# Performance work log

Measured on AMD Instinct MI355X. Metric: run time of the kernel, lower is better.

The kernel has to match this reference:

```python
import jax, jax.numpy as jnp
import numpy as np


def setup_inputs() -> dict:
    key = jax.random.key(0)
    k1, k2 = jax.random.split(key)
    B, IN, OUT = 8192, 4096, 2048
    x = jax.random.normal(k1, (B, IN), dtype=jnp.float32)
    # kaiming_normal_ on a (1, IN, OUT) tensor: fan_in = IN*OUT (torch treats dim0 as out-ch),
    # but the exact init scale is irrelevant for a correctness baseline; use std ~ sqrt(2/fan_in).
    std = np.sqrt(2.0 / (IN * OUT)).astype(np.float32)
    weight = jax.random.normal(k2, (1, IN, OUT), dtype=jnp.float32) * std
    return {"x": x, "weight": weight}


def reference(x, weight):
    # Faithful math: out[b, o] = sqrt(sum_i (x[b, i] - w[i, o])^2)
    # avoids the [B, IN, OUT] broadcast intermediate the torch code materializes).
    w = weight[0]                                   # [IN, OUT]
    x2 = jnp.sum(x * x, axis=1, keepdims=True)      # [B, 1]
    w2 = jnp.sum(w * w, axis=0, keepdims=True)      # [1, OUT]
    xw = jnp.matmul(x, w)                           # [B, OUT]
    d2 = x2 - 2.0 * xw + w2
    return jnp.sqrt(jnp.maximum(d2, 0.0))           # clamp tiny negative roundoff
```

## Files before the change

### kernel.cpp

```cpp
#include <hip/hip_runtime.h>


static constexpr int Mdim = 8192;
static constexpr int Ndim = 2048;
static constexpr int Kdim = 4096;

#define TILE_M 128
#define TILE_N 128
#define TILE_K 32

typedef float f32x4 __attribute__((ext_vector_type(4)));
typedef short s16x8 __attribute__((ext_vector_type(8)));
typedef __attribute__((address_space(3))) unsigned int lds_u32;
typedef const __attribute__((address_space(1))) unsigned int glb_u32;

__device__ __forceinline__ unsigned short f2bf(float f) {
    unsigned int u = __float_as_uint(f);
    return (unsigned short)((u + 0x7fffu + ((u >> 16) & 1u)) >> 16);
}

__global__ void prep_x_kernel(const float* __restrict__ x,
                              unsigned short* __restrict__ xb,
                              float* __restrict__ x2) {
    const int row = blockIdx.x;
    const int tid = threadIdx.x;
    const float4* xr = (const float4*)(x + (size_t)row * Kdim);
    ushort4* xo = (ushort4*)(xb + (size_t)row * Kdim);
    float ss = 0.f;
#pragma unroll
    for (int j = 0; j < 4; ++j) {
        float4 v = xr[j * 256 + tid];
        ss += v.x * v.x + v.y * v.y + v.z * v.z + v.w * v.w;
        ushort4 o;
        o.x = f2bf(v.x); o.y = f2bf(v.y); o.z = f2bf(v.z); o.w = f2bf(v.w);
        xo[j * 256 + tid] = o;
    }
#pragma unroll
    for (int d = 32; d >= 1; d >>= 1) ss += __shfl_down(ss, d, 64);
    __shared__ float ps[4];
    if ((tid & 63) == 0) ps[tid >> 6] = ss;
    __syncthreads();
    if (tid == 0) x2[row] = ps[0] + ps[1] + ps[2] + ps[3];
}

__global__ void prep_wt_kernel(const float* __restrict__ w,
                               unsigned short* __restrict__ wb,
                               float* __restrict__ w2) {
    __shared__ float t[64][65];
    const int tid = threadIdx.x;
    const int c0 = blockIdx.x * 64;
    const int r0 = blockIdx.y * 64;
#pragma unroll
    for (int p = 0; p < 4; ++p) {
        const int r = p * 16 + (tid >> 4);
        const int c = (tid & 15) * 4;
        float4 v = *(const float4*)(w + (size_t)(r0 + r) * Ndim + c0 + c);
        t[r][c] = v.x; t[r][c + 1] = v.y; t[r][c + 2] = v.z; t[r][c + 3] = v.w;
    }
    __syncthreads();
#pragma unroll
    for (int p = 0; p < 2; ++p) {
        const int o  = p * 32 + (tid >> 3);
        const int kc = (tid & 7) * 8;
        float ss = 0.f;
        ushort4 a, b;
        float v;
        v = t[kc + 0][o]; ss += v * v; a.x = f2bf(v);
        v = t[kc + 1][o]; ss += v * v; a.y = f2bf(v);
        v = t[kc + 2][o]; ss += v * v; a.z = f2bf(v);
        v = t[kc + 3][o]; ss += v * v; a.w = f2bf(v);
        v = t[kc + 4][o]; ss += v * v; b.x = f2bf(v);
        v = t[kc + 5][o]; ss += v * v; b.y = f2bf(v);
        v = t[kc + 6][o]; ss += v * v; b.z = f2bf(v);
        v = t[kc + 7][o]; ss += v * v; b.w = f2bf(v);
        ushort4* dst = (ushort4*)(wb + (size_t)(c0 + o) * Kdim + r0 + kc);
        dst[0] = a; dst[1] = b;
        ss += __shfl_xor(ss, 1, 64);
        ss += __shfl_xor(ss, 2, 64);
        ss += __shfl_xor(ss, 4, 64);
        if ((tid & 7) == 0) atomicAdd(&w2[c0 + o], ss);
    }
}

__global__ __launch_bounds__(256, 2) void gemm_dist_kernel(
    const unsigned short* __restrict__ Xb,
    const unsigned short* __restrict__ Wb,
    const float* __restrict__ x2,
    const float* __restrict__ w2,
    float* __restrict__ out)
{
    __shared__ __align__(16) unsigned char lds[2][16384];
    const int tid = threadIdx.x;
    const int lane = tid & 63;
    const int wid = tid >> 6;
    const int wr = wid >> 1, wc = wid & 1;

    const int nt_n = Ndim / TILE_N;
    const int nwg = (Mdim / TILE_M) * nt_n;
    const int q = nwg >> 3;
    const int swz = (blockIdx.x & 7) * q + (blockIdx.x >> 3);
    const int bm0 = (swz / nt_n) * TILE_M;
    const int bn0 = (swz % nt_n) * TILE_N;

    int srcA[2], srcB[2];
#pragma unroll
    for (int j = 0; j < 2; ++j) {
        int chunk = j * 256 + tid;
        int row = chunk >> 2;
        int scir = (chunk ^ row) & 3;
        srcA[j] = (bm0 + row) * Kdim + scir * 8;
        srcB[j] = (bn0 + row) * Kdim + scir * 8;
    }

    int aoff[4], boff[4];
#pragma unroll
    for (int m = 0; m < 4; ++m) {
        int ra = wr * 64 + m * 16 + (lane & 15);
        aoff[m] = ra * 64 + ((((lane >> 4) ^ ra) & 3) << 4);
        int rb = wc * 64 + m * 16 + (lane & 15);
        boff[m] = 8192 + rb * 64 + ((((lane >> 4) ^ rb) & 3) << 4);
    }

    f32x4 acc[4][4];
#pragma unroll
    for (int m = 0; m < 4; ++m)
#pragma unroll
        for (int n = 0; n < 4; ++n) acc[m][n] = (f32x4){0.f, 0.f, 0.f, 0.f};

    auto stage = [&](int bufi, int kt) {
        const unsigned short* ga0 = Xb + srcA[0] + kt * TILE_K;
        const unsigned short* ga1 = Xb + srcA[1] + kt * TILE_K;
        const unsigned short* gb0 = Wb + srcB[0] + kt * TILE_K;
        const unsigned short* gb1 = Wb + srcB[1] + kt * TILE_K;
        unsigned char* base = &lds[bufi][0];
        __builtin_amdgcn_global_load_lds((glb_u32*)ga0, (lds_u32*)(base + wid * 1024), 16, 0, 0);
        __builtin_amdgcn_global_load_lds((glb_u32*)ga1, (lds_u32*)(base + 4096 + wid * 1024), 16, 0, 0);
        __builtin_amdgcn_global_load_lds((glb_u32*)gb0, (lds_u32*)(base + 8192 + wid * 1024), 16, 0, 0);
        __builtin_amdgcn_global_load_lds((glb_u32*)gb1, (lds_u32*)(base + 8192 + 4096 + wid * 1024), 16, 0, 0);
    };

    stage(0, 0);
    __syncthreads();

    const int NT = Kdim / TILE_K;
    for (int kt = 0; kt < NT; ++kt) {
        const int cur = kt & 1;
        if (kt + 1 < NT) stage(cur ^ 1, kt + 1);
        const unsigned char* buf = &lds[cur][0];
        s16x8 af[4], bf[4];
#pragma unroll
        for (int m = 0; m < 4; ++m) af[m] = *(const s16x8*)(buf + aoff[m]);
#pragma unroll
        for (int n = 0; n < 4; ++n) bf[n] = *(const s16x8*)(buf + boff[n]);
#pragma unroll
        for (int m = 0; m < 4; ++m)
#pragma unroll
            for (int n = 0; n < 4; ++n)
                acc[m][n] = __builtin_amdgcn_mfma_f32_16x16x32_bf16(af[m], bf[n], acc[m][n], 0, 0, 0);
        __syncthreads();
    }

    const int col0 = bn0 + wc * 64 + (lane & 15);
    const int rb0 = bm0 + wr * 64 + ((lane >> 4) << 2);
    float w2v[4];
#pragma unroll
    for (int n = 0; n < 4; ++n) w2v[n] = w2[col0 + n * 16];
#pragma unroll
    for (int m = 0; m < 4; ++m) {
#pragma unroll
        for (int i = 0; i < 4; ++i) {
            const int row = rb0 + m * 16 + i;
            const float xv = x2[row];
#pragma unroll
            for (int n = 0; n < 4; ++n) {
                float d2 = xv - 2.f * acc[m][n][i] + w2v[n];
                out[(size_t)row * Ndim + col0 + n * 16] = sqrtf(fmaxf(d2, 0.f));
            }
        }
    }
}

__global__ __launch_bounds__(256) void fallback_dist_kernel(
    const float* __restrict__ x, const float* __restrict__ w, float* __restrict__ out)
{
    __shared__ float xs[16][65];
    __shared__ float wsd[16][65];
    const int tid = threadIdx.x;
    const int m0 = blockIdx.y * 64;
    const int n0 = blockIdx.x * 64;
    const int tx = tid & 15, ty = tid >> 4;
    float acc[4][4] = {};
    for (int k0 = 0; k0 < Kdim; k0 += 16) {
        __syncthreads();
#pragma unroll
        for (int p = 0; p < 4; ++p) {
            int idx = p * 256 + tid;
            int kk = idx >> 6, c = idx & 63;
            xs[kk][c] = x[(size_t)(m0 + c) * Kdim + k0 + kk];
            wsd[kk][c] = w[(size_t)(k0 + kk) * Ndim + n0 + c];
        }
        __syncthreads();
#pragma unroll
        for (int kk = 0; kk < 16; ++kk) {
            float a[4], b[4];
#pragma unroll
            for (int i = 0; i < 4; ++i) a[i] = xs[kk][ty * 4 + i];
#pragma unroll
            for (int j = 0; j < 4; ++j) b[j] = wsd[kk][tx * 4 + j];
#pragma unroll
            for (int i = 0; i < 4; ++i)
#pragma unroll
                for (int j = 0; j < 4; ++j) {
                    float d = a[i] - b[j];
                    acc[i][j] += d * d;
                }
        }
    }
#pragma unroll
    for (int i = 0; i < 4; ++i)
#pragma unroll
        for (int j = 0; j < 4; ++j)
            out[(size_t)(m0 + ty * 4 + i) * Ndim + n0 + tx * 4 + j] = sqrtf(acc[i][j]);
}

extern "C" void kernel_launch(void* const* d_in, const int* in_sizes, int n_in,
                              void* d_out, int out_size, void* d_ws, size_t ws_size,
                              hipStream_t stream) {
    const float* x = (const float*)d_in[0];
    const float* w = (const float*)d_in[1];
    float* out = (float*)d_out;
    char* ws = (char*)d_ws;

    const size_t xb_bytes = (size_t)Mdim * Kdim * 2;
    const size_t wb_bytes = (size_t)Ndim * Kdim * 2;
    const size_t need = xb_bytes + wb_bytes + (Mdim + Ndim) * sizeof(float);

    if (ws_size >= need) {
        unsigned short* Xb = (unsigned short*)(ws);
        unsigned short* Wb = (unsigned short*)(ws + xb_bytes);
        float* x2 = (float*)(ws + xb_bytes + wb_bytes);
        float* w2 = x2 + Mdim;

        hipMemsetAsync(w2, 0, Ndim * sizeof(float), stream);
        prep_x_kernel<<<Mdim, 256, 0, stream>>>(x, Xb, x2);
        prep_wt_kernel<<<dim3(Ndim / 64, Kdim / 64), 256, 0, stream>>>(w, Wb, w2);
        const int nwg = (Mdim / TILE_M) * (Ndim / TILE_N);
        gemm_dist_kernel<<<nwg, 256, 0, stream>>>(Xb, Wb, x2, w2, out);
    } else {
        fallback_dist_kernel<<<dim3(Ndim / 64, Mdim / 64), 256, 0, stream>>>(x, w, out);
    }
}
```

Measured before the change: 391.9 us.

## Enlarge GEMM tiles to 256x256 with 4-slot LDS pipeline and 8 waves

Raises the block tile to 256x256 with 512 threads, so each wave computes a 128x64 sub-tile. This raises arithmetic intensity per LDS and global byte. It replaces double buffering with a 4-slot ring that keeps three tiles in flight, using explicit vmcnt waits and s_barrier, and raises wave priority around the MFMA block. The costs are 128KB of LDS per block, which can rule out two blocks per CU despite the launch bounds, only 256 workgroups for the whole GPU, and higher register pressure from 32 accumulators.

```diff
diff --git a/kernel.cpp b/kernel.cpp
--- a/kernel.cpp
+++ b/kernel.cpp
@@ -5,9 +5,10 @@
 static constexpr int Ndim = 2048;
 static constexpr int Kdim = 4096;
 
-#define TILE_M 128
-#define TILE_N 128
-#define TILE_K 32
+#define BM 256
+#define BN 256
+#define BK 32
+#define NSLOT 4
 
 typedef float f32x4 __attribute__((ext_vector_type(4)));
 typedef short s16x8 __attribute__((ext_vector_type(8)));
@@ -82,99 +83,112 @@
     }
 }
 
-__global__ __launch_bounds__(256, 2) void gemm_dist_kernel(
+__global__ __launch_bounds__(512, 2) void gemm_dist_kernel(
     const unsigned short* __restrict__ Xb,
     const unsigned short* __restrict__ Wb,
     const float* __restrict__ x2,
     const float* __restrict__ w2,
     float* __restrict__ out)
 {
-    __shared__ __align__(16) unsigned char lds[2][16384];
+    __shared__ __align__(16) unsigned char lds[NSLOT][32768];
     const int tid = threadIdx.x;
     const int lane = tid & 63;
     const int wid = tid >> 6;
-    const int wr = wid >> 1, wc = wid & 1;
-
-    const int nt_n = Ndim / TILE_N;
-    const int nwg = (Mdim / TILE_M) * nt_n;
+    const int wr = wid >> 2;
+    const int wcn = wid & 3;
+
+    const int nt_n = Ndim / BN;
+    const int nwg = (Mdim / BM) * nt_n;
     const int q = nwg >> 3;
-    const int swz = (blockIdx.x & 7) * q + (blockIdx.x >> 3);
-    const int bm0 = (swz / nt_n) * TILE_M;
-    const int bn0 = (swz % nt_n) * TILE_N;
+    const int swz = ((int)blockIdx.x & 7) * q + ((int)blockIdx.x >> 3);
+    const int bm0 = (swz / nt_n) * BM;
+    const int bn0 = (swz % nt_n) * BN;
 
     int srcA[2], srcB[2];
 #pragma unroll
     for (int j = 0; j < 2; ++j) {
-        int chunk = j * 256 + tid;
-        int row = chunk >> 2;
-        int scir = (chunk ^ row) & 3;
-        srcA[j] = (bm0 + row) * Kdim + scir * 8;
-        srcB[j] = (bn0 + row) * Kdim + scir * 8;
-    }
-
-    int aoff[4], boff[4];
-#pragma unroll
-    for (int m = 0; m < 4; ++m) {
-        int ra = wr * 64 + m * 16 + (lane & 15);
-        aoff[m] = ra * 64 + ((((lane >> 4) ^ ra) & 3) << 4);
-        int rb = wc * 64 + m * 16 + (lane & 15);
-        boff[m] = 8192 + rb * 64 + ((((lane >> 4) ^ rb) & 3) << 4);
-    }
-
-    f32x4 acc[4][4];
-#pragma unroll
-    for (int m = 0; m < 4; ++m)
-#pragma unroll
-        for (int n = 0; n < 4; ++n) acc[m][n] = (f32x4){0.f, 0.f, 0.f, 0.f};
-
-    auto stage = [&](int bufi, int kt) {
-        const unsigned short* ga0 = Xb + srcA[0] + kt * TILE_K;
-        const unsigned short* ga1 = Xb + srcA[1] + kt * TILE_K;
-        const unsigned short* gb0 = Wb + srcB[0] + kt * TILE_K;
-        const unsigned short* gb1 = Wb + srcB[1] + kt * TILE_K;
-        unsigned char* base = &lds[bufi][0];
-        __builtin_amdgcn_global_load_lds((glb_u32*)ga0, (lds_u32*)(base + wid * 1024), 16, 0, 0);
-        __builtin_amdgcn_global_load_lds((glb_u32*)ga1, (lds_u32*)(base + 4096 + wid * 1024), 16, 0, 0);
-        __builtin_amdgcn_global_load_lds((glb_u32*)gb0, (lds_u32*)(base + 8192 + wid * 1024), 16, 0, 0);
-        __builtin_amdgcn_global_load_lds((glb_u32*)gb1, (lds_u32*)(base + 8192 + 4096 + wid * 1024), 16, 0, 0);
+        int c = wid * 128 + j * 64 + lane;
+        int lr = c >> 3, sc = c & 7;
+        int us = sc ^ (lr & 7);
+        int r = lr + ((us >> 2) << 7);
+        int cir = us & 3;
+        srcA[j] = (bm0 + r) * Kdim + cir * 8;
+        srcB[j] = (bn0 + r) * Kdim + cir * 8;
+    }
+
+    const int aconst = (lane & 15) * 128 +
+                       ((((wr << 2) | (lane >> 4)) ^ (lane & 7)) << 4);
+    const int bconst = 16384 + ((wcn & 1) * 64 + (lane & 15)) * 128 +
+                       (((((wcn >> 1) << 2) | (lane >> 4)) ^ (lane & 7)) << 4);
+
+    f32x4 acc[8][4];
+#pragma unroll
+    for (int mi = 0; mi < 8; ++mi)
+#pragma unroll
+        for (int ni = 0; ni < 4; ++ni) acc[mi][ni] = (f32x4){0.f, 0.f, 0.f, 0.f};
+
+    auto stage_tile = [&](int tt) {
+        unsigned char* sb = &lds[0][0] + (tt & 3) * 32768;
+        const int ko = tt * BK;
+#pragma unroll
+        for (int j = 0; j < 2; ++j) {
+            __builtin_amdgcn_global_load_lds((glb_u32*)(Xb + srcA[j] + ko),
+                (lds_u32*)(sb + wid * 2048 + j * 1024), 16, 0, 0);
+            __builtin_amdgcn_global_load_lds((glb_u32*)(Wb + srcB[j] + ko),
+                (lds_u32*)(sb + 16384 + wid * 2048 + j * 1024), 16, 0, 0);
+        }
     };
 
-    stage(0, 0);
-    __syncthreads();
-
-    const int NT = Kdim / TILE_K;
-    for (int kt = 0; kt < NT; ++kt) {
-        const int cur = kt & 1;
-        if (kt + 1 < NT) stage(cur ^ 1, kt + 1);
-        const unsigned char* buf = &lds[cur][0];
-        s16x8 af[4], bf[4];
-#pragma unroll
-        for (int m = 0; m < 4; ++m) af[m] = *(const s16x8*)(buf + aoff[m]);
-#pragma unroll
-        for (int n = 0; n < 4; ++n) bf[n] = *(const s16x8*)(buf + boff[n]);
-#pragma unroll
-        for (int m = 0; m < 4; ++m)
-#pragma unroll
-            for (int n = 0; n < 4; ++n)
-                acc[m][n] = __builtin_amdgcn_mfma_f32_16x16x32_bf16(af[m], bf[n], acc[m][n], 0, 0, 0);
-        __syncthreads();
-    }
-
-    const int col0 = bn0 + wc * 64 + (lane & 15);
-    const int rb0 = bm0 + wr * 64 + ((lane >> 4) << 2);
+    auto compute_slot = [&](int s) {
+        const unsigned char* sb = &lds[0][0] + s * 32768;
+        s16x8 a[8], b[4];
+#pragma unroll
+        for (int mi = 0; mi < 8; ++mi) a[mi] = *(const s16x8*)(sb + aconst + mi * 2048);
+#pragma unroll
+        for (int ni = 0; ni < 4; ++ni) b[ni] = *(const s16x8*)(sb + bconst + ni * 2048);
+        __builtin_amdgcn_s_setprio(1);
+#pragma unroll
+        for (int mi = 0; mi < 8; ++mi)
+#pragma unroll
+            for (int ni = 0; ni < 4; ++ni)
+                acc[mi][ni] = __builtin_amdgcn_mfma_f32_16x16x32_bf16(a[mi], b[ni], acc[mi][ni], 0, 0, 0);
+        __builtin_amdgcn_s_setprio(0);
+    };
+
+    stage_tile(0); stage_tile(1); stage_tile(2);
+
+    const int NT = Kdim / BK;
+    for (int t = 0; t < NT - 3; ++t) {
+        asm volatile("s_waitcnt vmcnt(8) lgkmcnt(0)" ::: "memory");
+        asm volatile("s_barrier" ::: "memory");
+        stage_tile(t + 3);
+        compute_slot(t & 3);
+    }
+    asm volatile("s_waitcnt vmcnt(8) lgkmcnt(0)" ::: "memory");
+    asm volatile("s_barrier" ::: "memory");
+    compute_slot((NT - 3) & 3);
+    asm volatile("s_waitcnt vmcnt(4) lgkmcnt(0)" ::: "memory");
+    asm volatile("s_barrier" ::: "memory");
+    compute_slot((NT - 2) & 3);
+    asm volatile("s_waitcnt vmcnt(0) lgkmcnt(0)" ::: "memory");
+    asm volatile("s_barrier" ::: "memory");
+    compute_slot((NT - 1) & 3);
+
+    const int col0 = bn0 + wcn * 64 + (lane & 15);
+    const int rb0 = bm0 + wr * 128 + ((lane >> 4) << 2);
     float w2v[4];
 #pragma unroll
-    for (int n = 0; n < 4; ++n) w2v[n] = w2[col0 + n * 16];
-#pragma unroll
-    for (int m = 0; m < 4; ++m) {
+    for (int ni = 0; ni < 4; ++ni) w2v[ni] = w2[col0 + ni * 16];
+#pragma unroll
+    for (int mi = 0; mi < 8; ++mi) {
 #pragma unroll
         for (int i = 0; i < 4; ++i) {
-            const int row = rb0 + m * 16 + i;
+            const int row = rb0 + mi * 16 + i;
             const float xv = x2[row];
 #pragma unroll
-            for (int n = 0; n < 4; ++n) {
-                float d2 = xv - 2.f * acc[m][n][i] + w2v[n];
-                out[(size_t)row * Ndim + col0 + n * 16] = sqrtf(fmaxf(d2, 0.f));
+            for (int ni = 0; ni < 4; ++ni) {
+                float d2 = xv - 2.f * acc[mi][ni][i] + w2v[ni];
+                out[(size_t)row * Ndim + col0 + ni * 16] = sqrtf(fmaxf(d2, 0.f));
             }
         }
     }
@@ -244,8 +258,8 @@
         hipMemsetAsync(w2, 0, Ndim * sizeof(float), stream);
         prep_x_kernel<<<Mdim, 256, 0, stream>>>(x, Xb, x2);
         prep_wt_kernel<<<dim3(Ndim / 64, Kdim / 64), 256, 0, stream>>>(w, Wb, w2);
-        const int nwg = (Mdim / TILE_M) * (Ndim / TILE_N);
-        gemm_dist_kernel<<<nwg, 256, 0, stream>>>(Xb, Wb, x2, w2, out);
+        const int nwg = (Mdim / BM) * (Ndim / BN);
+        gemm_dist_kernel<<<nwg, 512, 0, stream>>>(Xb, Wb, x2, w2, out);
     } else {
         fallback_dist_kernel<<<dim3(Ndim / 64, Mdim / 64), 256, 0, stream>>>(x, w, out);
     }
```

Measured after the change: 348.8 us. 11.0% less time.
